# Kernel optimization log

Hardware: AMD Instinct MI355X
Metric: run time of the kernel (lower is better)

The kernel has to match this reference:

```python
import jax, jax.numpy as jnp
import numpy as np

D = 512       # feature dim of X0 (Linear(512,...) in emb)
DQK = D // 8  # SAGAN-style reduced query/key dim
B = 256
S = 255       # structured features -> N = S + 1 tokens


def _lin(key, fan_in, fan_out):
    kw, kb = jax.random.split(key)
    s = 1.0 / np.sqrt(fan_in)
    W = jax.random.uniform(kw, (fan_in, fan_out), jnp.float32, -s, s)
    b = jax.random.uniform(kb, (fan_out,), jnp.float32, -s, s)
    return W, b


def setup_inputs() -> dict:
    key = jax.random.key(0)
    ks = jax.random.split(key, 9)
    X0 = jax.random.normal(ks[0], (B, D), jnp.float32)
    X_struc = jax.random.normal(ks[1], (B, S), jnp.float32)
    Wq, bq = _lin(ks[2], D, DQK)
    Wk, bk = _lin(ks[3], D, DQK)
    Wv, bv = _lin(ks[4], D, D)
    gamma = jnp.zeros((), jnp.float32) + 0.5  # nonzero so attention path contributes
    W1, b1 = _lin(ks[5], D, 1024)
    W2, b2 = _lin(ks[6], 1024, 512)
    W3, b3 = _lin(ks[7], 512, 128)
    return {"X0": X0, "X_struc": X_struc, "Wq": Wq, "bq": bq, "Wk": Wk, "bk": bk,
            "Wv": Wv, "bv": bv, "gamma": gamma, "W1": W1, "b1": b1,
            "W2": W2, "b2": b2, "W3": W3, "b3": b3}


def reference(X0, X_struc, Wq, bq, Wk, bk, Wv, bv, gamma, W1, b1, W2, b2, W3, b3):
    # Batched outer product replaces the per-sample torch.mm loop:
    # X1[b, s, d] = X_struc[b, s] * X0[b, d]
    X1 = X_struc[:, :, None] * X0[:, None, :]            # [B, S, D]
    X = jnp.concatenate([X0[:, None, :], X1], axis=1)    # [B, N, D], N = S+1
    # SAGAN-style self-attention (Self_Attention(out_planes=512))
    Q = X @ Wq + bq                                      # [B, N, DQK]
    K = X @ Wk + bk                                      # [B, N, DQK]
    V = X @ Wv + bv                                      # [B, N, D]
    A = jax.nn.softmax(jnp.einsum('bnc,bmc->bnm', Q, K), axis=-1)  # [B, N, N]
    Y = gamma * jnp.einsum('bnm,bmd->bnd', A, V) + X     # residual
    # emb MLP: 512 -> 1024 -> 512 -> 128, ReLU after each layer
    h = jax.nn.relu(Y @ W1 + b1)
    h = jax.nn.relu(h @ W2 + b2)
    out = jax.nn.relu(h @ W3 + b3)                       # [B, N, 128]
    return out
```

## Files before the change

kernel.cpp:

```cpp
#include <hip/hip_runtime.h>
#include <hip/hip_bf16.h>

typedef __attribute__((ext_vector_type(8))) short s16x8;
typedef __attribute__((ext_vector_type(16))) float f32x16;

__device__ __forceinline__ unsigned short f2bfu(float x) {
  __hip_bfloat16 b = __float2bfloat16(x);
  return *reinterpret_cast<unsigned short*>(&b);
}

__device__ __forceinline__ unsigned int cvtpk(float a, float b) {
  unsigned int r;
  asm("v_cvt_pk_bf16_f32 %0, %1, %2" : "=v"(r) : "v"(a), "v"(b));
  return r;
}

__global__ __launch_bounds__(256) void prep1_k(
    const float* __restrict__ W2, const float* __restrict__ W3,
    const float* __restrict__ W1,
    unsigned short* __restrict__ W2P, unsigned short* __restrict__ W3P,
    unsigned short* __restrict__ W1P,
    const float* __restrict__ X0, const float* __restrict__ Wv,
    const float* __restrict__ Wq, const float* __restrict__ Wk,
    float* __restrict__ V0ws, float* __restrict__ QKws) {
  __shared__ __align__(16) char smc[65664];
  const int tid = threadIdx.x;
  const int blk = blockIdx.x;

  if (blk < 64) {
    unsigned short* lt = (unsigned short*)smc;
    if (blk < 32) {
      const int kb = blk;
#pragma unroll
      for (int i = 0; i < 16; ++i) {
        const int e4 = i * 256 + tid;
        const int r = e4 >> 7, c4 = (e4 & 127) * 4;
        const float4 v = *(const float4*)(W2 + (size_t)(kb * 32 + r) * 512 + c4);
        lt[r * 514 + c4 + 0] = f2bfu(v.x);
        lt[r * 514 + c4 + 1] = f2bfu(v.y);
        lt[r * 514 + c4 + 2] = f2bfu(v.z);
        lt[r * 514 + c4 + 3] = f2bfu(v.w);
      }
      __syncthreads();
#pragma unroll
      for (int i = 0; i < 8; ++i) {
        const int c = i * 256 + tid;
        const int kgl = c >> 10, nb = (c >> 6) & 15, l = c & 63;
        const int col = nb * 32 + (l & 31);
        const int k0 = kgl * 16 + (l >> 5) * 8;
        s16x8 v;
#pragma unroll
        for (int j = 0; j < 8; ++j) v[j] = lt[(k0 + j) * 514 + col];
        *(s16x8*)(W2P + ((size_t)((kb * 2 + kgl) * 16 + nb) * 64 + l) * 8) = v;
      }
    } else if (blk < 48) {
      const int kb = blk - 32;
#pragma unroll
      for (int i = 0; i < 32; ++i) {
        const int e4 = i * 256 + tid;
        const int r = e4 >> 8, c4 = (e4 & 255) * 4;
        const float4 v = *(const float4*)(W1 + (size_t)(kb * 32 + r) * 1024 + c4);
        lt[r * 1026 + c4 + 0] = f2bfu(v.x);
        lt[r * 1026 + c4 + 1] = f2bfu(v.y);
        lt[r * 1026 + c4 + 2] = f2bfu(v.z);
        lt[r * 1026 + c4 + 3] = f2bfu(v.w);
      }
      __syncthreads();
#pragma unroll
      for (int i = 0; i < 16; ++i) {
        const int c = i * 256 + tid;
        const int kgl = c >> 11, nb = (c >> 6) & 31, l = c & 63;
        const int col = nb * 32 + (l & 31);
        const int k0 = kgl * 16 + (l >> 5) * 8;
        s16x8 v;
#pragma unroll
        for (int j = 0; j < 8; ++j) v[j] = lt[(k0 + j) * 1026 + col];
        *(s16x8*)(W1P + ((size_t)((kb * 2 + kgl) * 32 + nb) * 64 + l) * 8) = v;
      }
    } else {
      const int kb = blk - 48;
#pragma unroll
      for (int i = 0; i < 4; ++i) {
        const int e4 = i * 256 + tid;
        const int r = e4 >> 5, c4 = (e4 & 31) * 4;
        const float4 v = *(const float4*)(W3 + (size_t)(kb * 32 + r) * 128 + c4);
        lt[r * 130 + c4 + 0] = f2bfu(v.x);
        lt[r * 130 + c4 + 1] = f2bfu(v.y);
        lt[r * 130 + c4 + 2] = f2bfu(v.z);
        lt[r * 130 + c4 + 3] = f2bfu(v.w);
      }
      __syncthreads();
#pragma unroll
      for (int i = 0; i < 2; ++i) {
        const int c = i * 256 + tid;
        const int kgl = c >> 8, nb = (c >> 6) & 3, l = c & 63;
        const int col = nb * 32 + (l & 31);
        const int k0 = kgl * 16 + (l >> 5) * 8;
        s16x8 v;
#pragma unroll
        for (int j = 0; j < 8; ++j) v[j] = lt[(k0 + j) * 130 + col];
        *(s16x8*)(W3P + ((size_t)((kb * 2 + kgl) * 4 + nb) * 64 + l) * 8) = v;
      }
    }
    return;
  }
  float* As = (float*)smc;
  float* Bs = (float*)(smc + 2176);
  const int r = blk - 64;
  const int bn = r % 10, bm = r / 10;
  const int tx = tid & 15, ty = tid >> 4;
  float acc[2][4] = {};
  for (int k0 = 0; k0 < 512; k0 += 16) {
    if (tid < 128) {
      const int row = tid >> 2, kk = (tid & 3) * 4;
      const float4 v = *(const float4*)(X0 + (size_t)(bm * 32 + row) * 512 + k0 + kk);
      As[row * 17 + kk] = v.x; As[row * 17 + kk + 1] = v.y;
      As[row * 17 + kk + 2] = v.z; As[row * 17 + kk + 3] = v.w;
    }
    {
      const int k = tid >> 4, n4 = (tid & 15) * 4;
      float4 v;
      if (bn < 8)       v = *(const float4*)(Wv + (size_t)(k0 + k) * 512 + bn * 64 + n4);
      else if (bn == 8) v = *(const float4*)(Wq + (size_t)(k0 + k) * 64 + n4);
      else              v = *(const float4*)(Wk + (size_t)(k0 + k) * 64 + n4);
      Bs[k * 68 + n4] = v.x; Bs[k * 68 + n4 + 1] = v.y;
      Bs[k * 68 + n4 + 2] = v.z; Bs[k * 68 + n4 + 3] = v.w;
    }
    __syncthreads();
#pragma unroll
    for (int kk = 0; kk < 16; ++kk) {
      float a[2], bb[4];
#pragma unroll
      for (int i = 0; i < 2; ++i) a[i] = As[(ty * 2 + i) * 17 + kk];
#pragma unroll
      for (int j = 0; j < 4; ++j) bb[j] = Bs[kk * 68 + tx * 4 + j];
#pragma unroll
      for (int i = 0; i < 2; ++i)
#pragma unroll
        for (int j = 0; j < 4; ++j) acc[i][j] = fmaf(a[i], bb[j], acc[i][j]);
    }
    __syncthreads();
  }
#pragma unroll
  for (int i = 0; i < 2; ++i) {
    const int row = bm * 32 + ty * 2 + i;
#pragma unroll
    for (int j = 0; j < 4; ++j) {
      const int n = tx * 4 + j;
      if (bn < 8)       V0ws[(size_t)row * 512 + bn * 64 + n] = acc[i][j];
      else if (bn == 8) QKws[(size_t)row * 128 + n] = acc[i][j];
      else              QKws[(size_t)row * 128 + 64 + n] = acc[i][j];
    }
  }
}

__global__ __launch_bounds__(256) void prep2_k(
    const float* __restrict__ Xs, const float* __restrict__ QKws,
    const float* __restrict__ bq, float* __restrict__ Wws,
    const float* __restrict__ V0ws, const float* __restrict__ X0,
    const float* __restrict__ bv, const float* __restrict__ W1,
    const unsigned short* __restrict__ W1P,
    const float* __restrict__ gp, const float* __restrict__ b1,
    float* __restrict__ Pws, float* __restrict__ Rws, float* __restrict__ Cws) {
  const int tid = threadIdx.x;
  if (blockIdx.x < 256) {
    const int b = blockIdx.x, t = tid;
    __shared__ float sv[256];
    __shared__ float scal[4];
    sv[t] = (t == 0) ? 1.0f : Xs[b * 255 + t - 1];
    __syncthreads();
    if (t == 0) {
      float al = 0, g2 = 0;
      for (int j = 0; j < 64; ++j) {
        al = fmaf(QKws[b * 128 + j], QKws[b * 128 + 64 + j], al);
        g2 = fmaf(bq[j], QKws[b * 128 + 64 + j], g2);
      }
      float mx = sv[0], mn = sv[0];
      for (int m2 = 1; m2 < 256; ++m2) { mx = fmaxf(mx, sv[m2]); mn = fminf(mn, sv[m2]); }
      scal[0] = al; scal[1] = g2; scal[2] = mx; scal[3] = mn;
    }
    __syncthreads();
    const float c = fmaf(scal[0], sv[tid], scal[1]);
    const float M = (c >= 0.f) ? c * scal[2] : c * scal[3];
    float Z = 0, Wm = 0;
    for (int m2 = 0; m2 < 256; ++m2) {
      const float e = __expf(fmaf(c, sv[m2], -M));
      Z += e;
      Wm = fmaf(sv[m2], e, Wm);
    }
    Wws[b * 256 + tid] = Wm / Z;
    return;
  }
  if (blockIdx.x < 260) {
    const int col = (blockIdx.x - 256) * 256 + tid;
    float a = 0;
    for (int d = 0; d < 512; ++d) a = fmaf(bv[d], W1[(size_t)d * 1024 + col], a);
    Cws[col] = fmaf(gp[0], a, b1[col]);
    return;
  }
  const int r = blockIdx.x - 260;
  const int pr = r >> 6;
  const int rem = r & 63;
  const int mb = rem >> 4, nb = rem & 15;
  const float* srcA = pr ? X0 : V0ws;
  float* dst = pr ? Rws : Pws;
  const int lane = tid & 63, w = tid >> 6;
  const int la31 = lane & 31, hi = lane >> 5;
  const int rowbase = mb * 64 + (w >> 1) * 32;
  const int nbW = nb * 2 + (w & 1);
  const float* ar = srcA + (size_t)(rowbase + la31) * 512 + hi * 8;
  const unsigned short* pBW = W1P + ((size_t)nbW * 64 + lane) * 8;

  f32x16 acc;
#pragma unroll
  for (int i = 0; i < 16; ++i) acc[i] = 0.f;

  float4 fa[2][2];
  s16x8 bst[2];
  fa[0][0] = *(const float4*)(ar);
  fa[0][1] = *(const float4*)(ar + 4);
  bst[0] = *(const s16x8*)(pBW);
  pBW += 16384;

#pragma unroll 2
  for (int kg = 0; kg < 32; ++kg) {
    const int par = kg & 1;
    if (kg < 31) {
      fa[par ^ 1][0] = *(const float4*)(ar + (kg + 1) * 16);
      fa[par ^ 1][1] = *(const float4*)(ar + (kg + 1) * 16 + 4);
      bst[par ^ 1] = *(const s16x8*)(pBW);
      pBW += 16384;
    }
    union { s16x8 v; unsigned int u[4]; } t;
    const float4 a0 = fa[par][0], a1 = fa[par][1];
    t.u[0] = cvtpk(a0.x, a0.y);
    t.u[1] = cvtpk(a0.z, a0.w);
    t.u[2] = cvtpk(a1.x, a1.y);
    t.u[3] = cvtpk(a1.z, a1.w);
    acc = __builtin_amdgcn_mfma_f32_32x32x16_bf16(t.v, bst[par], acc, 0, 0, 0);
  }
#pragma unroll
  for (int reg = 0; reg < 16; ++reg) {
    const int rowl = (reg & 3) + 8 * (reg >> 2) + 4 * hi;
    dst[(size_t)(rowbase + rowl) * 1024 + nbW * 32 + la31] = acc[reg];
  }
}

__global__ __launch_bounds__(512, 2) void fused_k(
    const float* __restrict__ Xs, const float* __restrict__ gp,
    const unsigned short* __restrict__ W2P,
    const float* __restrict__ b2,
    const unsigned short* __restrict__ W3P,
    const float* __restrict__ b3,
    const float* __restrict__ Cws, const float* __restrict__ Wws,
    const float* __restrict__ Pws, const float* __restrict__ Rws,
    float* __restrict__ out)
{
  __shared__ __align__(16) unsigned char sm[143360];
  unsigned short* smU = (unsigned short*)sm;
  float* PRC = (float*)(sm + 131072);
  const int tid = threadIdx.x;
  const int lane = tid & 63, wid = tid >> 6;
  const int la31 = lane & 31, hi = lane >> 5;
  const int wr = wid >> 2, wc = wid & 3;
  const int m0 = blockIdx.x * 128;
  const int b = m0 >> 8;
  const float g = gp[0];

  float gwm[2], srm[2];
#pragma unroll
  for (int m = 0; m < 2; ++m) {
    const int tok = (m0 & 255) + wr * 64 + m * 32 + la31;
    gwm[m] = g * Wws[b * 256 + tok];
    srm[m] = (tok == 0) ? 1.0f : Xs[b * 255 + tok - 1];
  }

#pragma unroll
  for (int i = 0; i < 6; ++i) {
    const int idx = i * 512 + tid;
    float v;
    if (idx < 1024)      v = Pws[b * 1024 + idx];
    else if (idx < 2048) v = Rws[b * 1024 + (idx - 1024)];
    else                 v = Cws[idx - 2048];
    PRC[idx] = v;
  }

  f32x16 acc[2][4];
#pragma unroll
  for (int m = 0; m < 2; ++m)
#pragma unroll
    for (int n = 0; n < 4; ++n)
#pragma unroll
      for (int i = 0; i < 16; ++i) acc[m][n][i] = 0.f;

  const unsigned short* pB = W2P + ((size_t)(wc * 4) * 64 + lane) * 8;
  const float* Pp = PRC + hi * 8;
  s16x8 bst[2][4];
#pragma unroll
  for (int nf = 0; nf < 4; ++nf)
    bst[0][nf] = *(const s16x8*)(pB + nf * 512);
  pB += 8192;
  __syncthreads();

#pragma unroll 2
  for (int kg = 0; kg < 64; ++kg) {
    const int par = kg & 1;
#pragma unroll
    for (int nf = 0; nf < 4; ++nf)
      bst[par ^ 1][nf] = *(const s16x8*)(pB + nf * 512);
    pB += 8192;
    const float4 P0 = *(const float4*)(Pp + kg * 16);
    const float4 P1 = *(const float4*)(Pp + kg * 16 + 4);
    const float4 R0 = *(const float4*)(Pp + 1024 + kg * 16);
    const float4 R1 = *(const float4*)(Pp + 1024 + kg * 16 + 4);
    const float4 C0 = *(const float4*)(Pp + 2048 + kg * 16);
    const float4 C1 = *(const float4*)(Pp + 2048 + kg * 16 + 4);
    s16x8 af[2];
#pragma unroll
    for (int m = 0; m < 2; ++m) {
      const float gw = gwm[m], sr = srm[m];
      const float e0 = fmaxf(fmaf(gw, P0.x, fmaf(sr, R0.x, C0.x)), 0.f);
      const float e1 = fmaxf(fmaf(gw, P0.y, fmaf(sr, R0.y, C0.y)), 0.f);
      const float e2 = fmaxf(fmaf(gw, P0.z, fmaf(sr, R0.z, C0.z)), 0.f);
      const float e3 = fmaxf(fmaf(gw, P0.w, fmaf(sr, R0.w, C0.w)), 0.f);
      const float e4 = fmaxf(fmaf(gw, P1.x, fmaf(sr, R1.x, C1.x)), 0.f);
      const float e5 = fmaxf(fmaf(gw, P1.y, fmaf(sr, R1.y, C1.y)), 0.f);
      const float e6 = fmaxf(fmaf(gw, P1.z, fmaf(sr, R1.z, C1.z)), 0.f);
      const float e7 = fmaxf(fmaf(gw, P1.w, fmaf(sr, R1.w, C1.w)), 0.f);
      union { s16x8 v; unsigned int u[4]; } t;
      t.u[0] = cvtpk(e0, e1);
      t.u[1] = cvtpk(e2, e3);
      t.u[2] = cvtpk(e4, e5);
      t.u[3] = cvtpk(e6, e7);
      af[m] = t.v;
    }
#pragma unroll
    for (int nf = 0; nf < 4; ++nf)
#pragma unroll
      for (int m = 0; m < 2; ++m)
        acc[m][nf] = __builtin_amdgcn_mfma_f32_32x32x16_bf16(af[m], bst[par][nf], acc[m][nf], 0, 0, 0);
  }

#pragma unroll
  for (int nf = 0; nf < 4; ++nf) {
    const int col = wc * 128 + nf * 32 + la31;
    const float bb = b2[col];
    const int sc = col >> 3, c7 = col & 7;
#pragma unroll
    for (int m = 0; m < 2; ++m) {
#pragma unroll
      for (int reg = 0; reg < 16; ++reg) {
        const int row = wr * 64 + m * 32 + (reg & 3) + 8 * (reg >> 2) + 4 * hi;
        const int sp = (sc & 56) | ((sc ^ row) & 7);
        smU[row * 512 + sp * 8 + c7] = f2bfu(fmaxf(acc[m][nf][reg] + bb, 0.f));
      }
    }
  }
  __syncthreads();

  f32x16 acc2[2];
#pragma unroll
  for (int m = 0; m < 2; ++m)
#pragma unroll
    for (int i = 0; i < 16; ++i) acc2[m][i] = 0.f;

  const unsigned short* pW = W3P + ((size_t)wc * 64 + lane) * 8;
  s16x8 wst[2];
  wst[0] = *(const s16x8*)(pW);
  pW += 2048;
#pragma unroll 2
  for (int kg = 0; kg < 32; ++kg) {
    const int par = kg & 1;
    wst[par ^ 1] = *(const s16x8*)(pW);
    pW += 2048;
    const int s = kg * 2 + hi;
#pragma unroll
    for (int m = 0; m < 2; ++m) {
      const int row = wr * 64 + m * 32 + la31;
      const int sp = (s & 56) | ((s ^ row) & 7);
      const s16x8 afh = *(const s16x8*)(&sm[row * 1024 + (sp << 4)]);
      acc2[m] = __builtin_amdgcn_mfma_f32_32x32x16_bf16(afh, wst[par], acc2[m], 0, 0, 0);
    }
  }

  {
    const int cB = wc * 32 + la31;
    const float b3v = b3[cB];
#pragma unroll
    for (int m = 0; m < 2; ++m)
#pragma unroll
      for (int reg = 0; reg < 16; ++reg) {
        const int row = m0 + wr * 64 + m * 32 + (reg & 3) + 8 * (reg >> 2) + 4 * hi;
        out[(size_t)row * 128 + cB] = fmaxf(acc2[m][reg] + b3v, 0.f);
      }
  }
}

extern "C" void kernel_launch(void* const* d_in, const int* in_sizes, int n_in,
                              void* d_out, int out_size, void* d_ws, size_t ws_size,
                              hipStream_t stream) {
  const float* X0 = (const float*)d_in[0];
  const float* Xs = (const float*)d_in[1];
  const float* Wq = (const float*)d_in[2];
  const float* bq = (const float*)d_in[3];
  const float* Wk = (const float*)d_in[4];
  const float* bk = (const float*)d_in[5];
  const float* Wv = (const float*)d_in[6];
  const float* bv = (const float*)d_in[7];
  const float* gp = (const float*)d_in[8];
  const float* W1 = (const float*)d_in[9];
  const float* b1 = (const float*)d_in[10];
  const float* W2 = (const float*)d_in[11];
  const float* b2 = (const float*)d_in[12];
  const float* W3 = (const float*)d_in[13];
  const float* b3 = (const float*)d_in[14];

  char* ws = (char*)d_ws;
  float* Cws = (float*)(ws);
  float* Wws = (float*)(ws + 4096);
  float* Pws = (float*)(ws + 266240);
  float* Rws = (float*)(ws + 1314816);
  unsigned short* W2P = (unsigned short*)(ws + 2363392);
  unsigned short* W3P = (unsigned short*)(ws + 3411968);
  float* V0ws = (float*)(ws + 3543040);
  float* QKws = (float*)(ws + 4067328);
  unsigned short* W1P = (unsigned short*)(ws + 4198400);
  float* out = (float*)d_out;

  hipLaunchKernelGGL(prep1_k, dim3(144), dim3(256), 0, stream,
                     W2, W3, W1, W2P, W3P, W1P, X0, Wv, Wq, Wk, V0ws, QKws);
  hipLaunchKernelGGL(prep2_k, dim3(388), dim3(256), 0, stream,
                     Xs, QKws, bq, Wws, V0ws, X0, bv, W1, W1P, gp, b1, Pws, Rws, Cws);
  hipLaunchKernelGGL(fused_k, dim3(512), dim3(512), 0, stream,
                     Xs, gp, W2P, b2, W3P, b3, Cws, Wws, Pws, Rws, out);
}
```

Before: 146.2 us.

## Remap layer-2 GEMM warps to full-M 128x64 tiles per wave

Layer-2 work is re-split across the 8 waves. Each wave now covers all 128 rows and a 64-column slice (4x2 MFMA fragments) instead of a 64x128 tile (2x4). This halves the per-wave W2 fragment loads from global memory but doubles the on-the-fly activation recompute and conversion per wave (4 A fragments instead of 2). The layer-3 stage keeps the old warp mapping.

```diff
diff --git a/kernel.cpp b/kernel.cpp
--- a/kernel.cpp
+++ b/kernel.cpp
@@ -262,17 +262,16 @@
   const int tid = threadIdx.x;
   const int lane = tid & 63, wid = tid >> 6;
   const int la31 = lane & 31, hi = lane >> 5;
-  const int wr = wid >> 2, wc = wid & 3;
   const int m0 = blockIdx.x * 128;
   const int b = m0 >> 8;
   const float g = gp[0];
 
-  float gwm[2], srm[2];
-#pragma unroll
-  for (int m = 0; m < 2; ++m) {
-    const int tok = (m0 & 255) + wr * 64 + m * 32 + la31;
-    gwm[m] = g * Wws[b * 256 + tok];
-    srm[m] = (tok == 0) ? 1.0f : Xs[b * 255 + tok - 1];
+  float gwm[4], srm[4];
+#pragma unroll
+  for (int mf = 0; mf < 4; ++mf) {
+    const int tok = (m0 & 255) + mf * 32 + la31;
+    gwm[mf] = g * Wws[b * 256 + tok];
+    srm[mf] = (tok == 0) ? 1.0f : Xs[b * 255 + tok - 1];
   }
 
 #pragma unroll
@@ -285,19 +284,19 @@
     PRC[idx] = v;
   }
 
-  f32x16 acc[2][4];
-#pragma unroll
-  for (int m = 0; m < 2; ++m)
-#pragma unroll
-    for (int n = 0; n < 4; ++n)
-#pragma unroll
-      for (int i = 0; i < 16; ++i) acc[m][n][i] = 0.f;
-
-  const unsigned short* pB = W2P + ((size_t)(wc * 4) * 64 + lane) * 8;
+  f32x16 acc[4][2];
+#pragma unroll
+  for (int mf = 0; mf < 4; ++mf)
+#pragma unroll
+    for (int nf = 0; nf < 2; ++nf)
+#pragma unroll
+      for (int i = 0; i < 16; ++i) acc[mf][nf][i] = 0.f;
+
+  const unsigned short* pB = W2P + ((size_t)(wid * 2) * 64 + lane) * 8;
   const float* Pp = PRC + hi * 8;
-  s16x8 bst[2][4];
-#pragma unroll
-  for (int nf = 0; nf < 4; ++nf)
+  s16x8 bst[2][2];
+#pragma unroll
+  for (int nf = 0; nf < 2; ++nf)
     bst[0][nf] = *(const s16x8*)(pB + nf * 512);
   pB += 8192;
   __syncthreads();
@@ -306,7 +305,7 @@
   for (int kg = 0; kg < 64; ++kg) {
     const int par = kg & 1;
 #pragma unroll
-    for (int nf = 0; nf < 4; ++nf)
+    for (int nf = 0; nf < 2; ++nf)
       bst[par ^ 1][nf] = *(const s16x8*)(pB + nf * 512);
     pB += 8192;
     const float4 P0 = *(const float4*)(Pp + kg * 16);
@@ -315,10 +314,10 @@
     const float4 R1 = *(const float4*)(Pp + 1024 + kg * 16 + 4);
     const float4 C0 = *(const float4*)(Pp + 2048 + kg * 16);
     const float4 C1 = *(const float4*)(Pp + 2048 + kg * 16 + 4);
-    s16x8 af[2];
-#pragma unroll
-    for (int m = 0; m < 2; ++m) {
-      const float gw = gwm[m], sr = srm[m];
+    s16x8 af[4];
+#pragma unroll
+    for (int mf = 0; mf < 4; ++mf) {
+      const float gw = gwm[mf], sr = srm[mf];
       const float e0 = fmaxf(fmaf(gw, P0.x, fmaf(sr, R0.x, C0.x)), 0.f);
       const float e1 = fmaxf(fmaf(gw, P0.y, fmaf(sr, R0.y, C0.y)), 0.f);
       const float e2 = fmaxf(fmaf(gw, P0.z, fmaf(sr, R0.z, C0.z)), 0.f);
@@ -332,32 +331,33 @@
       t.u[1] = cvtpk(e2, e3);
       t.u[2] = cvtpk(e4, e5);
       t.u[3] = cvtpk(e6, e7);
-      af[m] = t.v;
-    }
-#pragma unroll
-    for (int nf = 0; nf < 4; ++nf)
-#pragma unroll
-      for (int m = 0; m < 2; ++m)
-        acc[m][nf] = __builtin_amdgcn_mfma_f32_32x32x16_bf16(af[m], bst[par][nf], acc[m][nf], 0, 0, 0);
-  }
-
-#pragma unroll
-  for (int nf = 0; nf < 4; ++nf) {
-    const int col = wc * 128 + nf * 32 + la31;
+      af[mf] = t.v;
+    }
+#pragma unroll
+    for (int nf = 0; nf < 2; ++nf)
+#pragma unroll
+      for (int mf = 0; mf < 4; ++mf)
+        acc[mf][nf] = __builtin_amdgcn_mfma_f32_32x32x16_bf16(af[mf], bst[par][nf], acc[mf][nf], 0, 0, 0);
+  }
+
+#pragma unroll
+  for (int nf = 0; nf < 2; ++nf) {
+    const int col = wid * 64 + nf * 32 + la31;
     const float bb = b2[col];
     const int sc = col >> 3, c7 = col & 7;
 #pragma unroll
-    for (int m = 0; m < 2; ++m) {
+    for (int mf = 0; mf < 4; ++mf) {
 #pragma unroll
       for (int reg = 0; reg < 16; ++reg) {
-        const int row = wr * 64 + m * 32 + (reg & 3) + 8 * (reg >> 2) + 4 * hi;
+        const int row = mf * 32 + (reg & 3) + 8 * (reg >> 2) + 4 * hi;
         const int sp = (sc & 56) | ((sc ^ row) & 7);
-        smU[row * 512 + sp * 8 + c7] = f2bfu(fmaxf(acc[m][nf][reg] + bb, 0.f));
+        smU[row * 512 + sp * 8 + c7] = f2bfu(fmaxf(acc[mf][nf][reg] + bb, 0.f));
       }
     }
   }
   __syncthreads();
 
+  const int wr = wid >> 2, wc = wid & 3;
   f32x16 acc2[2];
 #pragma unroll
   for (int m = 0; m < 2; ++m)
```

Result: slower. 156.0 us (+6.7%).
